# Kernel optimization log

Measured on AMD Instinct MI355X. Metric: run time of the kernel, lower is better.

The kernel has to match this reference:

```python
import jax, jax.numpy as jnp
import numpy as np

TIMESTEPS = 1000
DIFFUSION_SPEED = 0.01
B, N = 4, 2048
E = N * (N - 1) // 2  # strict lower-triangular entries per graph


def _build_Qt():
    # Qt[t-1] = [[1-f, f], [f, 1-f]],  f = 0.5*(1-(1-2s)^t), t = 1..T
    ts = jnp.arange(1, TIMESTEPS + 1, dtype=jnp.float32)
    flip = 0.5 * (1.0 - (1.0 - 2.0 * DIFFUSION_SPEED) ** ts)          # [T]
    row0 = jnp.stack([1.0 - flip, flip], axis=-1)                      # [T,2]
    row1 = jnp.stack([flip, 1.0 - flip], axis=-1)                      # [T,2]
    return jnp.stack([row0, row1], axis=1)                             # [T,2,2]


def setup_inputs() -> dict:
    key = jax.random.key(0)
    k1, k2, k3, k4 = jax.random.split(key, 4)
    adj_start = jax.random.randint(k1, (B, N, N), 0, 2, dtype=jnp.int32)
    t = jax.random.randint(k2, (B,), 0, TIMESTEPS, dtype=jnp.int32)
    u = jax.random.uniform(k3, (B, N, N), dtype=jnp.float32)
    q_approx = jax.random.normal(k4, (B, E), dtype=jnp.float32)
    return {"adj_start": adj_start, "t": t, "u": u, "q_approx": q_approx}


def reference(adj_start, t, u, q_approx):
    Qt = _build_Qt()                                                   # [T,2,2]
    # symmetrize raw adjacency into a binary undirected adjacency
    a = jnp.tril(adj_start, -1)
    adj0 = a + jnp.swapaxes(a, -1, -2)                                 # [B,N,N] in {0,1}

    b_idx = jnp.arange(B)[:, None, None]

    # ---- forward diffusion: sample x_t ~ Categorical(Qt[t][adj0]) ----
    probs = Qt[t][b_idx, adj0]                                         # [B,N,N,2]
    x_t = (u < probs[..., 1]).astype(adj0.dtype)                       # [B,N,N]

    # ---- backward diffusion: q(x_{t-1} | x_t, x_0) ----
    Q_likelihood = Qt[0]                                               # [2,2]
    Q_prior = Qt[t - 1]                                                # [B,2,2] (t=0 wraps, as in torch)
    Q_evidence = Qt[t]                                                 # [B,2,2]

    likelihood = Q_likelihood[x_t]                                     # [B,N,N,2]
    prior = Q_prior[b_idx, adj0]                                       # [B,N,N,2]
    evidence = Q_evidence[b_idx, adj0, x_t]                            # [B,N,N]
    q_backward = likelihood * prior / evidence[..., None]              # [B,N,N,2]

    ti, tj = np.tril_indices(N, -1)                                    # static indices
    q_target = q_backward[:, ti, tj, 1]                                # [B,E]

    # ---- BCE-with-logits loss (mean) ----
    x = q_approx
    loss = jnp.mean(jnp.maximum(x, 0.0) - x * q_target + jnp.log1p(jnp.exp(-jnp.abs(x))))
    return loss
```

## Files before the change

### kernel.cpp

```cpp
#include <hip/hip_runtime.h>
#include <math.h>

#define TIMESTEPS 1000
constexpr int Bc = 4;
constexpr int Nc = 2048;
constexpr int EcI = Nc * (Nc - 1) / 2;
constexpr int EG  = EcI / 4;

__global__ __launch_bounds__(256) void diff_loss_kernel(
    const int* __restrict__ adj, const int* __restrict__ t,
    const float* __restrict__ u, const float* __restrict__ q,
    double* __restrict__ partials)
{
    __shared__ float tab[Bc][8];
    if (threadIdx.x < Bc) {
        int b = threadIdx.x;
        int tb = t[b];
        float f_t = 0.5f * (1.0f - powf(0.98f, (float)(tb + 1)));
        int tpe = (tb == 0) ? TIMESTEPS : tb;
        float f_p = 0.5f * (1.0f - powf(0.98f, (float)tpe));
        float f0  = 0.5f * (1.0f - 0.98f);
        float omf_t = 1.0f - f_t;
        tab[b][0] = f_t;
        tab[b][1] = omf_t;
        tab[b][2] = f0          * f_p          / omf_t;
        tab[b][3] = (1.0f - f0) * f_p          / f_t;
        tab[b][4] = f0          * (1.0f - f_p) / f_t;
        tab[b][5] = (1.0f - f0) * (1.0f - f_p) / omf_t;
    }
    __syncthreads();

    const int totalEG = Bc * EG;
    const int stride = gridDim.x * blockDim.x;
    double acc = 0.0;
    for (int g = blockIdx.x * blockDim.x + threadIdx.x; g < totalEG; g += stride) {
        int b  = g / EG;
        int e0 = (g - b * EG) << 2;

        float sf = sqrtf((float)(8 * e0 + 1));
        int i = (int)((1.0f + sf) * 0.5f);
        if (i * (i - 1) / 2 > e0)  --i;
        if (i * (i + 1) / 2 <= e0) ++i;
        int j = e0 - i * (i - 1) / 2;

        float p0   = tab[b][0], p1   = tab[b][1];
        float qt00 = tab[b][2], qt01 = tab[b][3];
        float qt10 = tab[b][4], qt11 = tab[b][5];

        const float4 q4 = *(const float4*)(q + b * EcI + e0);
        const float qk[4] = {q4.x, q4.y, q4.z, q4.w};

        int ii = i, jj = j;
        float s = 0.0f;
        #pragma unroll
        for (int k = 0; k < 4; ++k) {
            bool adv = (jj >= ii);
            ii += adv;
            jj = adv ? 0 : jj;
            int base = (b << 22) + (ii << 11) + jj;
            int   a0 = adj[base];
            float uu = u[base];
            float ps  = a0 ? p1 : p0;
            bool  x   = (uu < ps);
            float t0  = x ? qt01 : qt00;
            float t1  = x ? qt11 : qt10;
            float qtv = a0 ? t1 : t0;
            float qv  = qk[k];
            s += fmaxf(qv, 0.0f) - qv * qtv + __logf(1.0f + __expf(-fabsf(qv)));
            ++jj;
        }
        acc += (double)s;
    }

    for (int off = 32; off > 0; off >>= 1)
        acc += __shfl_down(acc, off, 64);
    __shared__ double wsum[4];
    int lane = threadIdx.x & 63, wid = threadIdx.x >> 6;
    if (lane == 0) wsum[wid] = acc;
    __syncthreads();
    if (threadIdx.x == 0)
        partials[blockIdx.x] = wsum[0] + wsum[1] + wsum[2] + wsum[3];
}

__global__ __launch_bounds__(256) void final_reduce_kernel(
    const double* __restrict__ partials, int nb, float* __restrict__ out)
{
    double acc = 0.0;
    for (int idx = threadIdx.x; idx < nb; idx += blockDim.x)
        acc += partials[idx];
    for (int off = 32; off > 0; off >>= 1)
        acc += __shfl_down(acc, off, 64);
    __shared__ double wsum[4];
    int lane = threadIdx.x & 63, wid = threadIdx.x >> 6;
    if (lane == 0) wsum[wid] = acc;
    __syncthreads();
    if (threadIdx.x == 0)
        out[0] = (float)((wsum[0] + wsum[1] + wsum[2] + wsum[3]) /
                         ((double)Bc * (double)EcI));
}

extern "C" void kernel_launch(void* const* d_in, const int* in_sizes, int n_in,
                              void* d_out, int out_size, void* d_ws, size_t ws_size,
                              hipStream_t stream) {
    const int*   adj = (const int*)d_in[0];
    const int*   t   = (const int*)d_in[1];
    const float* u   = (const float*)d_in[2];
    const float* q   = (const float*)d_in[3];
    float*  out      = (float*)d_out;
    double* partials = (double*)d_ws;

    const int NB = 2048;
    diff_loss_kernel<<<NB, 256, 0, stream>>>(adj, t, u, q, partials);
    final_reduce_kernel<<<1, 256, 0, stream>>>(partials, NB, out);
}
```

Measured before the change: 164.7 us.

## Fold lower triangle into rectangle with one coalesced element per thread

Replaces the grid-stride loop, in which each thread handled four consecutive triangle entries found by a float sqrt inversion, with a folded rectangle of 1024 x 2047 entries per graph. Row r pairs with row 2047-r, so each thread maps to one (i,j) with plain integer arithmetic. Consecutive lanes now read adjacent adj/u elements, giving coalesced loads and removing the sqrt and index fix-up. The cost is many more blocks (about 32K), a full double-precision wave reduction per single element, and a final reduce over far more partials.

```diff
diff --git a/kernel.cpp b/kernel.cpp
--- a/kernel.cpp
+++ b/kernel.cpp
@@ -5,7 +5,9 @@
 constexpr int Bc = 4;
 constexpr int Nc = 2048;
 constexpr int EcI = Nc * (Nc - 1) / 2;
-constexpr int EG  = EcI / 4;
+constexpr int VW = Nc - 1;
+constexpr int PerB = 1024 * VW;
+constexpr int Total = Bc * PerB;
 
 __global__ __launch_bounds__(256) void diff_loss_kernel(
     const int* __restrict__ adj, const int* __restrict__ t,
@@ -30,48 +32,35 @@
     }
     __syncthreads();
 
-    const int totalEG = Bc * EG;
-    const int stride = gridDim.x * blockDim.x;
-    double acc = 0.0;
-    for (int g = blockIdx.x * blockDim.x + threadIdx.x; g < totalEG; g += stride) {
-        int b  = g / EG;
-        int e0 = (g - b * EG) << 2;
+    const int g = blockIdx.x * blockDim.x + threadIdx.x;
+    int b   = g / PerB;
+    int rem = g - b * PerB;
+    int r   = rem / VW;
+    int c   = rem - r * VW;
 
-        float sf = sqrtf((float)(8 * e0 + 1));
-        int i = (int)((1.0f + sf) * 0.5f);
-        if (i * (i - 1) / 2 > e0)  --i;
-        if (i * (i + 1) / 2 <= e0) ++i;
-        int j = e0 - i * (i - 1) / 2;
+    bool lo = (c < r);
+    int i = lo ? r : (Nc - 1) - r;
+    int j = lo ? c : c - r;
 
-        float p0   = tab[b][0], p1   = tab[b][1];
-        float qt00 = tab[b][2], qt01 = tab[b][3];
-        float qt10 = tab[b][4], qt11 = tab[b][5];
+    int mbase = (b << 22) + (i << 11) + j;
+    int e     = ((i * (i - 1)) >> 1) + j;
 
-        const float4 q4 = *(const float4*)(q + b * EcI + e0);
-        const float qk[4] = {q4.x, q4.y, q4.z, q4.w};
+    int   a0 = adj[mbase];
+    float uu = u[mbase];
+    float qv = q[b * EcI + e];
 
-        int ii = i, jj = j;
-        float s = 0.0f;
-        #pragma unroll
-        for (int k = 0; k < 4; ++k) {
-            bool adv = (jj >= ii);
-            ii += adv;
-            jj = adv ? 0 : jj;
-            int base = (b << 22) + (ii << 11) + jj;
-            int   a0 = adj[base];
-            float uu = u[base];
-            float ps  = a0 ? p1 : p0;
-            bool  x   = (uu < ps);
-            float t0  = x ? qt01 : qt00;
-            float t1  = x ? qt11 : qt10;
-            float qtv = a0 ? t1 : t0;
-            float qv  = qk[k];
-            s += fmaxf(qv, 0.0f) - qv * qtv + __logf(1.0f + __expf(-fabsf(qv)));
-            ++jj;
-        }
-        acc += (double)s;
-    }
+    float p0   = tab[b][0], p1   = tab[b][1];
+    float qt00 = tab[b][2], qt01 = tab[b][3];
+    float qt10 = tab[b][4], qt11 = tab[b][5];
 
+    float ps  = a0 ? p1 : p0;
+    bool  x   = (uu < ps);
+    float t0  = x ? qt01 : qt00;
+    float t1  = x ? qt11 : qt10;
+    float qtv = a0 ? t1 : t0;
+    float s = fmaxf(qv, 0.0f) - qv * qtv + __logf(1.0f + __expf(-fabsf(qv)));
+
+    double acc = (double)s;
     for (int off = 32; off > 0; off >>= 1)
         acc += __shfl_down(acc, off, 64);
     __shared__ double wsum[4];
@@ -109,7 +98,7 @@
     float*  out      = (float*)d_out;
     double* partials = (double*)d_ws;
 
-    const int NB = 2048;
+    const int NB = Total / 256;
     diff_loss_kernel<<<NB, 256, 0, stream>>>(adj, t, u, q, partials);
     final_reduce_kernel<<<1, 256, 0, stream>>>(partials, NB, out);
 }
```

New measurement: 204.6 us. 24.2% more time.
